# Kernel tuning notes

Hardware: AMD Instinct MI355X
Metric: run time of the kernel (lower is better)

## Reference

```python
import jax, jax.numpy as jnp
import numpy as np

NEG = -1e30  # log(0) surrogate that stays finite in fp32
BLANK = 0


def setup_inputs() -> dict:
    key = jax.random.key(0)
    k1, k2 = jax.random.split(key)
    B, T, V, L = 32, 1024, 1024, 256
    logits = jax.random.normal(k1, (B, T, V), dtype=jnp.float32)
    log_probs = jax.nn.log_softmax(logits, axis=-1)  # module expects log-probs
    labels = jax.random.randint(k2, (B, L), 1, V, dtype=jnp.int32)  # avoid blank=0
    input_lens = jnp.full((B,), T, dtype=jnp.int32)
    label_lens = jnp.full((B,), L, dtype=jnp.int32)
    return {"log_probs": log_probs, "labels": labels,
            "input_lens": input_lens, "label_lens": label_lens}


def _ctc_loss_sum(log_probs, labels, input_lens, label_lens, blank=BLANK):
    """CTC forward DP (alpha recursion) in log space; reduction='sum', zero_infinity=True."""
    B, T, V = log_probs.shape
    L = labels.shape[1]
    S = 2 * L + 1  # extended label: blank l1 blank l2 ... blank

    ext = jnp.full((B, S), blank, dtype=labels.dtype)
    ext = ext.at[:, 1::2].set(labels)
    # skip transition s-2 -> s allowed iff ext[s] != blank and ext[s] != ext[s-2]
    skip = jnp.concatenate(
        [jnp.zeros((B, 2), dtype=bool),
         (ext[:, 2:] != blank) & (ext[:, 2:] != ext[:, :-2])], axis=1)

    lp_tbv = jnp.transpose(log_probs, (1, 0, 2))  # 'btv->tbv' as in the module

    emit0 = jnp.take_along_axis(lp_tbv[0], ext, axis=1)  # [B,S]
    alpha0 = jnp.full((B, S), NEG, dtype=log_probs.dtype)
    alpha0 = alpha0.at[:, 0].set(emit0[:, 0]).at[:, 1].set(emit0[:, 1])

    neg1 = jnp.full((B, 1), NEG, dtype=log_probs.dtype)
    neg2 = jnp.full((B, 2), NEG, dtype=log_probs.dtype)

    def step(alpha, inputs):
        lp_t, t = inputs  # lp_t: [B,V]
        em = jnp.take_along_axis(lp_t, ext, axis=1)  # [B,S]
        a1 = alpha
        a2 = jnp.concatenate([neg1, alpha[:, :-1]], axis=1)
        a3 = jnp.where(skip, jnp.concatenate([neg2, alpha[:, :-2]], axis=1), NEG)
        new = jnp.logaddexp(jnp.logaddexp(a1, a2), a3) + em
        # freeze alpha once past this sample's input length
        new = jnp.where((t < input_lens)[:, None], new, alpha)
        return new, None

    ts = jnp.arange(1, T)
    alpha, _ = jax.lax.scan(step, alpha0, (lp_tbv[1:], ts))

    s_last = 2 * label_lens  # final blank state index per sample
    a_last = jnp.take_along_axis(alpha, s_last[:, None], axis=1)[:, 0]
    a_prev = jnp.take_along_axis(alpha, (s_last - 1)[:, None], axis=1)[:, 0]
    loss_b = -jnp.logaddexp(a_last, a_prev)
    loss_b = jnp.where(loss_b > 1e29, 0.0, loss_b)  # zero_infinity=True
    return jnp.sum(loss_b)


def reference(log_probs, labels, input_lens, label_lens):
    return _ctc_loss_sum(log_probs, labels, input_lens, label_lens)
```

## Files before the change

kernel.cpp:

```cpp
#include <hip/hip_runtime.h>


constexpr int B_ = 32, T_ = 1024, V_ = 1024, L_ = 256;
constexpr int CH = 16;
constexpr int NCHUNK = 64;
constexpr float LN2F = 0.6931471805599453f;

typedef const __attribute__((address_space(1))) unsigned int* gp_t;
typedef __attribute__((address_space(3))) unsigned int* lp_t;

template <int CTRL>
__device__ __forceinline__ float dpp_fmax(float x) {
    const int t = __builtin_amdgcn_update_dpp(0, __float_as_int(x), CTRL, 0xf, 0xf, true);
    return fmaxf(x, __int_as_float(t));
}

__device__ __forceinline__ float wave_max_dpp(float x) {
    x = dpp_fmax<0x111>(x);
    x = dpp_fmax<0x112>(x);
    x = dpp_fmax<0x114>(x);
    x = dpp_fmax<0x118>(x);
    x = dpp_fmax<0x142>(x);
    x = dpp_fmax<0x143>(x);
    return __int_as_float(__builtin_amdgcn_readlane(__float_as_int(x), 63));
}

__device__ __forceinline__ float dpp_wave_shr1(float x) {
    return __int_as_float(
        __builtin_amdgcn_update_dpp(0, __float_as_int(x), 0x138, 0xf, 0xf, true));
}

__global__ __launch_bounds__(256, 8) void ctc_gather(
    const float* __restrict__ lp, float* __restrict__ qdst, int qstride,
    const int* __restrict__ labels, float* __restrict__ blanks)
{
    __shared__ float srow[4][V_];
    const int wave = threadIdx.x >> 6;
    const int lane = threadIdx.x & 63;
    const int r = blockIdx.x * 4 + wave;
    const int b = r >> 10;
    const float* row = lp + (size_t)r * V_;
    float* orow = qdst + (size_t)r * qstride;
    const int* labb = labels + b * L_;

    #pragma unroll
    for (int j = 0; j < 4; ++j)
        __builtin_amdgcn_global_load_lds((gp_t)(row + 256 * j + 4 * lane),
                                         (lp_t)&srow[wave][256 * j], 16, 0, 0);
    const int4 e = *(const int4*)(labb + 4 * lane);
    asm volatile("s_waitcnt vmcnt(0)" ::: "memory");
    __builtin_amdgcn_sched_barrier(0);
    const float v0 = srow[wave][e.x];
    const float v1 = srow[wave][e.y];
    const float v2 = srow[wave][e.z];
    const float v3 = srow[wave][e.w];
    const float vb = srow[wave][0];
    float4 q;
    q.x = __expf(v0); q.y = __expf(v1); q.z = __expf(v2); q.w = __expf(v3);
    const float qb = __expf(vb);
    *(float4*)(orow + 4 * lane) = q;
    if (lane == 0) {
        const int t = r & (T_ - 1);
        blanks[(r & ~(T_ - 1)) + ((t + T_ - 1) & (T_ - 1))] = qb;
    }
}

__global__ __launch_bounds__(64, 1) void ctc_dp(
    const float* __restrict__ Q, int qstride,
    const float* __restrict__ blanks, const int* __restrict__ labels,
    const int* __restrict__ input_lens, const int* __restrict__ label_lens,
    float* __restrict__ out)
{
    __shared__ float blk[T_];
    const int b    = blockIdx.x;
    const int lane = threadIdx.x & 63;
    const float* Qb  = Q + (size_t)b * T_ * qstride;
    const float* blg = blanks + b * T_;
    const int*  labb = labels + b * L_;
    const int il = input_lens[b];
    const int ll = label_lens[b];
    const int tend = il < T_ ? il : T_;

    #pragma unroll
    for (int i = 0; i < 4; ++i)
        __builtin_amdgcn_global_load_lds((gp_t)(blg + 256 * i + 4 * lane),
                                         (lp_t)&blk[256 * i], 16, 0, 0);

    const int4 e  = *(const int4*)(labb + 4 * lane);
    const int  ep = (lane > 0) ? labb[4 * lane - 1] : -1;
    const float kf0 = ((8 * lane + 1) >= 3 && e.x != ep) ? 1.f : 0.f;
    const float kf1 = (e.y != e.x) ? 1.f : 0.f;
    const float kf2 = (e.z != e.y) ? 1.f : 0.f;
    const float kf3 = (e.w != e.z) ? 1.f : 0.f;
    const float bl0 = blg[T_ - 1];
    const float q00 = Qb[0];
    float p0 = (lane == 0) ? bl0 : 0.f;
    float p1 = (lane == 0) ? q00 : 0.f;
    float p2 = 0.f, p3 = 0.f, p4 = 0.f, p5 = 0.f,
          p6 = 0.f, p7 = 0.f, p8 = 0.f;
    int Esc = 0;
    float pm1 = 0.f;
    float sfP = 1.f, sfM = 1.f;

    asm volatile("s_waitcnt vmcnt(0)" ::: "memory");
    __builtin_amdgcn_sched_barrier(0);

    auto snap = [&]() -> float {
        float m = fmaxf(fmaxf(fmaxf(fmaxf(p0, p1), fmaxf(p2, p3)),
                              fmaxf(fmaxf(p4, p5), fmaxf(p6, p7))), p8);
        m = wave_max_dpp(m);
        const unsigned eb = (__float_as_uint(m) >> 23) & 0xffu;
        if (eb >= 1u && eb <= 254u) {
            unsigned k = 318u - eb;
            if (k > 254u) k = 254u;
            Esc += (int)k - 127;
            return __uint_as_float(k << 23);
        }
        return 1.f;
    };

    auto qaddr = [&](int t) -> const float4* {
        return (const float4*)(Qb + (size_t)t * qstride + 4 * lane);
    };

    float4 qa[CH], qbf[CH];
    float4 bbA[4], bbB[4];
    #pragma unroll
    for (int i = 0; i < CH; ++i) { int t = 1 + i; qa[i] = *qaddr(t); }
    #pragma unroll
    for (int i = 0; i < CH; ++i) {
        int t = 1 + CH + i; if (t > T_ - 1) t = T_ - 1;
        qbf[i] = *qaddr(t);
    }
    #pragma unroll
    for (int j = 0; j < 4; ++j) bbA[j] = *(const float4*)&blk[4 * j];
    #pragma unroll
    for (int j = 0; j < 4; ++j) bbB[j] = *(const float4*)&blk[CH + 4 * j];

    auto compute_chunk = [&](int c, float4 (&qv)[CH], float4 (&bv)[4]) {
        #pragma unroll
        for (int i = 0; i < CH; ++i) {
            float4 q = qv[i];
            const int g = i & 3;
            const float4 f4 = bv[i >> 2];
            float qb = (g == 0) ? f4.x : (g == 1) ? f4.y
                     : (g == 2) ? f4.z : f4.w;
            if (i == 0) { q.x *= sfP; q.y *= sfP; q.z *= sfP; q.w *= sfP; qb *= sfP; }
            if (i == 8) { q.x *= sfM; q.y *= sfM; q.z *= sfM; q.w *= sfM; qb *= sfM; }
            const int t = 1 + c * CH + i;
            if (t < tend) {
                const float n7 = fmaf(kf3, p5, p7 + p6) * q.w;
                const float n8 = (p8 + p7) * qb;
                const float pm1n = dpp_wave_shr1(n7);
                const float n0 = (p0 + pm1) * qb;
                const float n1 = fmaf(kf0, pm1, p1 + p0) * q.x;
                const float n2 = (p2 + p1) * qb;
                const float n3 = fmaf(kf1, p1, p3 + p2) * q.y;
                const float n4 = (p4 + p3) * qb;
                const float n5 = fmaf(kf2, p3, p5 + p4) * q.z;
                const float n6 = (p6 + p5) * qb;
                p0 = n0; p1 = n1; p2 = n2; p3 = n3; p4 = n4;
                p5 = n5; p6 = n6; p7 = n7; p8 = n8; pm1 = pm1n;
            }
            if (i == 4)  sfM = snap();
            if (i == 12) sfP = snap();
        }
    };

    for (int c = 0; c < NCHUNK; c += 2) {
        compute_chunk(c, qa, bbA);
        if (c + 2 < NCHUNK) {
            #pragma unroll
            for (int i = 0; i < CH; ++i) {
                int t = 1 + (c + 2) * CH + i; if (t > T_ - 1) t = T_ - 1;
                qa[i] = *qaddr(t);
            }
            #pragma unroll
            for (int j = 0; j < 4; ++j)
                bbA[j] = *(const float4*)&blk[(c + 2) * CH + 4 * j];
        }
        compute_chunk(c + 1, qbf, bbB);
        if (c + 3 < NCHUNK) {
            #pragma unroll
            for (int i = 0; i < CH; ++i) {
                int t = 1 + (c + 3) * CH + i; if (t > T_ - 1) t = T_ - 1;
                qbf[i] = *qaddr(t);
            }
            #pragma unroll
            for (int j = 0; j < 4; ++j)
                bbB[j] = *(const float4*)&blk[(c + 3) * CH + 4 * j];
        }
    }
    p0 *= sfP; p1 *= sfP; p2 *= sfP; p3 *= sfP; p4 *= sfP;
    p5 *= sfP; p6 *= sfP; p7 *= sfP; p8 *= sfP;

    const int sl = 2 * ll;
    auto pick = [&](int s) -> float {
        if (s == 512) return __shfl(p8, 63);
        const int r = s & 7;
        float v = p0;
        v = (r == 1) ? p1 : v; v = (r == 2) ? p2 : v;
        v = (r == 3) ? p3 : v; v = (r == 4) ? p4 : v;
        v = (r == 5) ? p5 : v; v = (r == 6) ? p6 : v;
        v = (r == 7) ? p7 : v;
        return __shfl(v, s >> 3);
    };
    const float la = pick(sl);
    const float lb = pick(sl - 1);
    if (lane == 0) {
        const float tot = la + lb;
        float loss = (float)Esc * LN2F - __logf(tot);
        if (!(loss <= 1e29f)) loss = 0.f;
        atomicAdd(out, loss);
    }
}

extern "C" void kernel_launch(void* const* d_in, const int* in_sizes, int n_in,
                              void* d_out, int out_size, void* d_ws, size_t ws_size,
                              hipStream_t stream) {
    float*       lp     = (float*)d_in[0];
    const int*   labels = (const int*)d_in[1];
    const int*   il     = (const int*)d_in[2];
    const int*   ll     = (const int*)d_in[3];
    float* out    = (float*)d_out;
    float* blanks = (float*)d_ws;

    const size_t need = (size_t)B_ * T_ * sizeof(float)
                      + (size_t)B_ * T_ * 256 * sizeof(float);
    const bool use_ws = ws_size >= need;
    float* qdst = use_ws ? (blanks + (size_t)B_ * T_) : lp;
    const int qstride = use_ws ? 256 : V_;

    hipMemsetAsync(out, 0, sizeof(float), stream);
    ctc_gather<<<dim3(B_ * T_ / 4), dim3(256), 0, stream>>>(
        lp, qdst, qstride, labels, blanks);
    ctc_dp<<<dim3(B_), dim3(64), 0, stream>>>(
        qdst, qstride, blanks, labels, il, ll, out);
}
```

Before: 337.6 us.

## Stage DP emission chunks through LDS with a four-deep async prefetch ring

```diff
diff --git a/kernel.cpp b/kernel.cpp
--- a/kernel.cpp
+++ b/kernel.cpp
@@ -4,6 +4,7 @@
 constexpr int B_ = 32, T_ = 1024, V_ = 1024, L_ = 256;
 constexpr int CH = 16;
 constexpr int NCHUNK = 64;
+constexpr int NBUF = 4;
 constexpr float LN2F = 0.6931471805599453f;
 
 typedef const __attribute__((address_space(1))) unsigned int* gp_t;
@@ -72,6 +73,7 @@
     float* __restrict__ out)
 {
     __shared__ float blk[T_];
+    __shared__ float buf[NBUF][CH][256];
     const int b    = blockIdx.x;
     const int lane = threadIdx.x & 63;
     const float* Qb  = Q + (size_t)b * T_ * qstride;
@@ -81,10 +83,21 @@
     const int ll = label_lens[b];
     const int tend = il < T_ ? il : T_;
 
+    auto issue_chunk = [&](int c) {
+        #pragma unroll
+        for (int i = 0; i < CH; ++i) {
+            int t = 1 + c * CH + i; if (t > T_ - 1) t = T_ - 1;
+            __builtin_amdgcn_global_load_lds(
+                (gp_t)(Qb + (size_t)t * qstride + 4 * lane),
+                (lp_t)&buf[c & (NBUF - 1)][i][0], 16, 0, 0);
+        }
+    };
+
     #pragma unroll
     for (int i = 0; i < 4; ++i)
         __builtin_amdgcn_global_load_lds((gp_t)(blg + 256 * i + 4 * lane),
                                          (lp_t)&blk[256 * i], 16, 0, 0);
+    issue_chunk(0); issue_chunk(1); issue_chunk(2);
 
     const int4 e  = *(const int4*)(labb + 4 * lane);
     const int  ep = (lane > 0) ? labb[4 * lane - 1] : -1;
@@ -102,7 +115,7 @@
     float pm1 = 0.f;
     float sfP = 1.f, sfM = 1.f;
 
-    asm volatile("s_waitcnt vmcnt(0)" ::: "memory");
+    asm volatile("s_waitcnt vmcnt(32)" ::: "memory");
     __builtin_amdgcn_sched_barrier(0);
 
     auto snap = [&]() -> float {
@@ -119,32 +132,33 @@
         return 1.f;
     };
 
-    auto qaddr = [&](int t) -> const float4* {
-        return (const float4*)(Qb + (size_t)t * qstride + 4 * lane);
-    };
-
-    float4 qa[CH], qbf[CH];
-    float4 bbA[4], bbB[4];
-    #pragma unroll
-    for (int i = 0; i < CH; ++i) { int t = 1 + i; qa[i] = *qaddr(t); }
-    #pragma unroll
-    for (int i = 0; i < CH; ++i) {
-        int t = 1 + CH + i; if (t > T_ - 1) t = T_ - 1;
-        qbf[i] = *qaddr(t);
-    }
-    #pragma unroll
-    for (int j = 0; j < 4; ++j) bbA[j] = *(const float4*)&blk[4 * j];
-    #pragma unroll
-    for (int j = 0; j < 4; ++j) bbB[j] = *(const float4*)&blk[CH + 4 * j];
-
-    auto compute_chunk = [&](int c, float4 (&qv)[CH], float4 (&bv)[4]) {
+    for (int c = 0; c < NCHUNK; ++c) {
+        if (c + 3 < NCHUNK) {
+            issue_chunk(c + 3);
+            asm volatile("s_waitcnt vmcnt(32)" ::: "memory");
+        } else if (c == NCHUNK - 3) {
+            asm volatile("s_waitcnt vmcnt(16)" ::: "memory");
+        } else if (c == NCHUNK - 2) {
+            asm volatile("s_waitcnt vmcnt(0)"  ::: "memory");
+        }
+        __builtin_amdgcn_sched_barrier(0);
+
+        const float* base = &buf[c & (NBUF - 1)][0][0] + 4 * lane;
+        float4 qv[CH];
+        #pragma unroll
+        for (int i = 0; i < CH; ++i)
+            qv[i] = *(const float4*)(base + 256 * i);
+        float bb[CH];
+        #pragma unroll
+        for (int i = 0; i < CH; i += 4) {
+            const float4 t4 = *(const float4*)&blk[c * CH + i];
+            bb[i] = t4.x; bb[i + 1] = t4.y;
+            bb[i + 2] = t4.z; bb[i + 3] = t4.w;
+        }
         #pragma unroll
         for (int i = 0; i < CH; ++i) {
             float4 q = qv[i];
-            const int g = i & 3;
-            const float4 f4 = bv[i >> 2];
-            float qb = (g == 0) ? f4.x : (g == 1) ? f4.y
-                     : (g == 2) ? f4.z : f4.w;
+            float qb = bb[i];
             if (i == 0) { q.x *= sfP; q.y *= sfP; q.z *= sfP; q.w *= sfP; qb *= sfP; }
             if (i == 8) { q.x *= sfM; q.y *= sfM; q.z *= sfM; q.w *= sfM; qb *= sfM; }
             const int t = 1 + c * CH + i;
@@ -165,31 +179,6 @@
             if (i == 4)  sfM = snap();
             if (i == 12) sfP = snap();
         }
-    };
-
-    for (int c = 0; c < NCHUNK; c += 2) {
-        compute_chunk(c, qa, bbA);
-        if (c + 2 < NCHUNK) {
-            #pragma unroll
-            for (int i = 0; i < CH; ++i) {
-                int t = 1 + (c + 2) * CH + i; if (t > T_ - 1) t = T_ - 1;
-                qa[i] = *qaddr(t);
-            }
-            #pragma unroll
-            for (int j = 0; j < 4; ++j)
-                bbA[j] = *(const float4*)&blk[(c + 2) * CH + 4 * j];
-        }
-        compute_chunk(c + 1, qbf, bbB);
-        if (c + 3 < NCHUNK) {
-            #pragma unroll
-            for (int i = 0; i < CH; ++i) {
-                int t = 1 + (c + 3) * CH + i; if (t > T_ - 1) t = T_ - 1;
-                qbf[i] = *qaddr(t);
-            }
-            #pragma unroll
-            for (int j = 0; j < 4; ++j)
-                bbB[j] = *(const float4*)&blk[(c + 3) * CH + 4 * j];
-        }
     }
     p0 *= sfP; p1 *= sfP; p2 *= sfP; p3 *= sfP; p4 *= sfP;
     p5 *= sfP; p6 *= sfP; p7 *= sfP; p8 *= sfP;
```

Result: faster. 299.5 us (-11.3%).
